# Performance work log

Measured on AMD Instinct MI355X. Metric: run time of the kernel, lower is better.

Reference implementation:

```python
import jax, jax.numpy as jnp
import numpy as np

D_MODEL = 768
N_HEADS = 12
D_K = D_MODEL // N_HEADS
NEG_INF = -1e10


def setup_inputs() -> dict:
    key = jax.random.key(0)
    ks = jax.random.split(key, 12)
    B, S = 2, 4096
    scale = 1.0 / np.sqrt(D_MODEL)
    inp = {
        "q": jax.random.normal(ks[0], (B, S, D_MODEL), jnp.float32),
        "k": jax.random.normal(ks[1], (B, S, D_MODEL), jnp.float32),
        "v": jax.random.normal(ks[2], (B, S, D_MODEL), jnp.float32),
        "mask": jnp.ones((B, S), jnp.int32),
        "Wq": jax.random.normal(ks[3], (D_MODEL, D_MODEL), jnp.float32) * scale,
        "bq": jnp.zeros((D_MODEL,), jnp.float32),
        "Wk": jax.random.normal(ks[4], (D_MODEL, D_MODEL), jnp.float32) * scale,
        "bk": jnp.zeros((D_MODEL,), jnp.float32),
        "Wv": jax.random.normal(ks[5], (D_MODEL, D_MODEL), jnp.float32) * scale,
        "bv": jnp.zeros((D_MODEL,), jnp.float32),
        "Wo": jax.random.normal(ks[6], (D_MODEL, D_MODEL), jnp.float32) * scale,
        "bo": jnp.zeros((D_MODEL,), jnp.float32),
    }
    return inp


def reference(q, k, v, mask, Wq, bq, Wk, bk, Wv, bv, Wo, bo):
    B, Sq, _ = q.shape
    Sk = k.shape[1]
    # linear projections (flax Linear: x @ kernel + bias)
    query = q @ Wq + bq
    key_ = k @ Wk + bk
    value = v @ Wv + bv
    # split heads: [B, H, S, d_k]
    query = query.reshape(B, Sq, N_HEADS, D_K).transpose(0, 2, 1, 3)
    key_ = key_.reshape(B, Sk, N_HEADS, D_K).transpose(0, 2, 1, 3)
    value = value.reshape(B, Sk, N_HEADS, D_K).transpose(0, 2, 1, 3)
    # scores [B, H, Sq, Sk]
    scores = jnp.einsum('bhqd,bhkd->bhqk', query, key_) / jnp.sqrt(
        jnp.asarray(D_K, query.dtype))
    m = mask[:, None, None, :]  # 2D mask -> [B,1,1,Sk]
    scores = jnp.where(m == 0, NEG_INF, scores)
    attn = jax.nn.softmax(scores, axis=-1)
    # dropout deterministic (is_training=False): identity
    x = jnp.einsum('bhqk,bhkd->bhqd', attn, value)
    x = x.transpose(0, 2, 1, 3).reshape(B, Sq, D_MODEL)
    return x @ Wo + bo
```

## Files before the change

### kernel.cpp

```cpp
#include <hip/hip_runtime.h>

typedef __attribute__((ext_vector_type(8))) short short8;
typedef __attribute__((ext_vector_type(4))) float floatx4;
typedef __attribute__((ext_vector_type(16))) float floatx16;
typedef unsigned short ushort_t;

#define S_LEN 4096
#define NH 12
#define DK 64
#define DM 768
#define BQ 128
#define LOG2E 1.4426950408889634f

static __device__ __forceinline__ unsigned short f2bf(float f) {
    unsigned int u = __float_as_uint(f);
    u += 0x7FFFu + ((u >> 16) & 1u);
    return (unsigned short)(u >> 16);
}
static __device__ __forceinline__ unsigned pack2(float a, float b) {
    return (unsigned)f2bf(a) | ((unsigned)f2bf(b) << 16);
}
static __device__ __forceinline__ void gld_lds16(const void* g, void* l) {
    __builtin_amdgcn_global_load_lds(
        (__attribute__((address_space(1))) void*)g,
        (__attribute__((address_space(3))) void*)l, 16, 0, 0);
}

__global__ __launch_bounds__(256)
void wtrans_kernel(const float* __restrict__ W0, const float* __restrict__ W1,
                   const float* __restrict__ W2, const float* __restrict__ W3,
                   ushort_t* __restrict__ T0, ushort_t* __restrict__ T1,
                   ushort_t* __restrict__ T2, ushort_t* __restrict__ T3) {
    __shared__ float tile[32][33];
    const int z = blockIdx.z;
    const float* W = (z == 0) ? W0 : (z == 1) ? W1 : (z == 2) ? W2 : W3;
    ushort_t* T = (z == 0) ? T0 : (z == 1) ? T1 : (z == 2) ? T2 : T3;
    const int bx = blockIdx.x, by = blockIdx.y;
    const int tx = threadIdx.x, ty = threadIdx.y;
    #pragma unroll
    for (int j = 0; j < 32; j += 8)
        tile[ty + j][tx] = W[(size_t)(by * 32 + ty + j) * DM + bx * 32 + tx];
    __syncthreads();
    #pragma unroll
    for (int j = 0; j < 32; j += 8)
        T[(size_t)(bx * 32 + ty + j) * DM + by * 32 + tx] = f2bf(tile[tx][ty + j]);
}

__global__ __launch_bounds__(256)
void cvt_kernel(const float* __restrict__ A0, const float* __restrict__ A1,
                const float* __restrict__ A2, ushort_t* __restrict__ O0,
                ushort_t* __restrict__ O1, ushort_t* __restrict__ O2) {
    const int z = blockIdx.y;
    const float* A = (z == 0) ? A0 : (z == 1) ? A1 : A2;
    ushort_t* O = (z == 0) ? O0 : (z == 1) ? O1 : O2;
    const size_t i = ((size_t)blockIdx.x * 256 + threadIdx.x) * 8;
    const float4 f0 = *(const float4*)(A + i);
    const float4 f1 = *(const float4*)(A + i + 4);
    uint4 o;
    o.x = pack2(f0.x, f0.y);
    o.y = pack2(f0.z, f0.w);
    o.z = pack2(f1.x, f1.y);
    o.w = pack2(f1.z, f1.w);
    *(uint4*)(O + i) = o;
}

__global__ __launch_bounds__(256)
void vtrans_kernel(const ushort_t* __restrict__ Vn, ushort_t* __restrict__ Vt) {
    __shared__ ushort_t tl[64 * 72];
    const int s0 = blockIdx.x * 64;
    const size_t bh = blockIdx.y;
    const int t = threadIdx.x;
    {
        const int r = t >> 2, c0 = (t & 3) * 16;
        const uint4* src = (const uint4*)(Vn + (bh * S_LEN + s0 + r) * DK + c0);
        uint4 a0 = src[0], a1 = src[1];
        uint4* dst = (uint4*)&tl[r * 72 + c0];
        dst[0] = a0;
        dst[1] = a1;
    }
    __syncthreads();
    {
        const int d = t >> 2, c0 = (t & 3) * 16;
        alignas(16) ushort_t tmp[16];
        #pragma unroll
        for (int j = 0; j < 16; ++j) tmp[j] = tl[(c0 + j) * 72 + d];
        uint4* dst = (uint4*)(Vt + (bh * DK + d) * S_LEN + s0 + c0);
        dst[0] = *(const uint4*)&tmp[0];
        dst[1] = *(const uint4*)&tmp[8];
    }
}

struct GemmArgs {
    const ushort_t* A[3];
    const ushort_t* Wt[3];
    const float* bias[3];
    void* C[3];
    float scale[3];
};

template <int MODE>
__global__ __launch_bounds__(256, 3)
void gemm_kernel(GemmArgs args) {
    __shared__ ushort_t As[128 * 32];
    __shared__ ushort_t Bs[128 * 32];
    const int z = blockIdx.z;
    const ushort_t* A = args.A[z];
    const ushort_t* Wt = args.Wt[z];
    const float* bias = args.bias[z];
    void* Carg = args.C[z];
    const float scale = args.scale[z];

    const int m0 = blockIdx.x * 128;
    const int n0 = blockIdx.y * 128;
    const int t = threadIdx.x;
    const int w = t >> 6, lane = t & 63, l15 = lane & 15, quad = lane >> 4;
    const int rowoff = (w >> 1) * 64, coloff = (w & 1) * 64;
    const int srow = w * 16 + (lane >> 2);
    const int scol = (lane & 3) * 8;

    floatx4 acc[4][4];
    #pragma unroll
    for (int i = 0; i < 4; ++i)
        #pragma unroll
        for (int j = 0; j < 4; ++j) acc[i][j] = (floatx4){0.f, 0.f, 0.f, 0.f};

    for (int kt = 0; kt < DM; kt += 32) {
        __syncthreads();
        #pragma unroll
        for (int j = 0; j < 2; ++j) {
            const int r = j * 64 + srow;
            gld_lds16(A + (size_t)(m0 + r) * DM + kt + scol, &As[r * 32 + scol]);
            gld_lds16(Wt + (size_t)(n0 + r) * DM + kt + scol, &Bs[r * 32 + scol]);
        }
        __asm__ __volatile__("s_waitcnt vmcnt(0)" ::: "memory");
        __syncthreads();
        short8 af[4], bfr[4];
        #pragma unroll
        for (int i = 0; i < 4; ++i)
            af[i] = *(const short8*)&As[(rowoff + 16 * i + l15) * 32 + quad * 8];
        #pragma unroll
        for (int j = 0; j < 4; ++j)
            bfr[j] = *(const short8*)&Bs[(coloff + 16 * j + l15) * 32 + quad * 8];
        #pragma unroll
        for (int i = 0; i < 4; ++i)
            #pragma unroll
            for (int j = 0; j < 4; ++j)
                acc[i][j] = __builtin_amdgcn_mfma_f32_16x16x32_bf16(af[i], bfr[j], acc[i][j], 0, 0, 0);
    }

    #pragma unroll
    for (int i = 0; i < 4; ++i) {
        #pragma unroll
        for (int j = 0; j < 4; ++j) {
            #pragma unroll
            for (int reg = 0; reg < 4; ++reg) {
                const int m = m0 + rowoff + 16 * i + quad * 4 + reg;
                const int n = n0 + coloff + 16 * j + l15;
                const float v2 = (acc[i][j][reg] + bias[n]) * scale;
                if (MODE == 0) {
                    ushort_t* Out = (ushort_t*)Carg;
                    const int b = m >> 12, s = m & 4095, h = n >> 6, d = n & 63;
                    Out[((size_t)((b * NH + h) * S_LEN + s)) * DK + d] = f2bf(v2);
                } else {
                    float* Out = (float*)Carg;
                    Out[(size_t)m * DM + n] = v2;
                }
            }
        }
    }
}

__global__ __launch_bounds__(256, 3)
void attn_kernel(const ushort_t* __restrict__ Q, const ushort_t* __restrict__ K,
                 const ushort_t* __restrict__ VT, const int* __restrict__ mask,
                 ushort_t* __restrict__ X) {
    __shared__ ushort_t Qs[BQ * DK];
    __shared__ ushort_t Ks0[64 * DK], Ks1[64 * DK];
    __shared__ ushort_t Vs0[64 * DK], Vs1[64 * DK];

    const int id = blockIdx.x;
    const int per = id >> 3;
    const int bh = (id & 7) * 3 + (per >> 5);
    const int qb = per & 31;
    const int b = bh / NH, h = bh - b * NH;
    const size_t bho = (size_t)bh * S_LEN;
    const ushort_t* Vbase = VT + (size_t)bh * DK * S_LEN;
    const int t = threadIdx.x;
    const int w = t >> 6, lane = t & 63, l31 = lane & 31, half = lane >> 5;
    const int q0 = qb * BQ;
    const int swl = l31 & 7;
    const int frow8 = lane >> 3;
    const int fcc = lane & 7;

    auto fillK = [&](int kv0, ushort_t* Kb) {
        #pragma unroll
        for (int j = 0; j < 2; ++j) {
            const int r = (w * 2 + j) * 8 + frow8;
            const int c8 = fcc ^ (r & 7);
            gld_lds16(K + (bho + kv0 + r) * DK + c8 * 8, &Kb[r * DK + fcc * 8]);
        }
    };
    auto fillV = [&](int kv0, ushort_t* Vb) {
        #pragma unroll
        for (int j = 0; j < 2; ++j) {
            const int r = (w * 2 + j) * 8 + frow8;
            const int c8 = fcc ^ (r & 7);
            gld_lds16(Vbase + (size_t)r * S_LEN + kv0 + c8 * 8, &Vb[r * DK + fcc * 8]);
        }
    };

    fillK(0, Ks0);
    fillV(0, Vs0);
    #pragma unroll
    for (int j = 0; j < 4; ++j) {
        const int r = (w * 4 + j) * 8 + frow8;
        const int c8 = fcc ^ (r & 7);
        gld_lds16(Q + (bho + q0 + r) * DK + c8 * 8, &Qs[r * DK + fcc * 8]);
    }
    int ok = 1;
    {
        const int* mrow = mask + (size_t)b * S_LEN + t * 16;
        #pragma unroll
        for (int i = 0; i < 4; ++i) {
            const int4 mm = *(const int4*)(mrow + i * 4);
            ok &= (mm.x != 0) & (mm.y != 0) & (mm.z != 0) & (mm.w != 0);
        }
    }
    const int allones = __syncthreads_and(ok);

    short8 qf[4];
    #pragma unroll
    for (int ks = 0; ks < 4; ++ks) {
        const int c8 = ks * 2 + half;
        qf[ks] = *(const short8*)&Qs[(w * 32 + l31) * DK + ((c8 ^ swl) << 3)];
    }

    floatx16 o[2];
    #pragma unroll
    for (int dt = 0; dt < 2; ++dt)
        #pragma unroll
        for (int r = 0; r < 16; ++r) o[dt][r] = 0.f;
    float l_r = 0.f;

    auto body = [&](int it, const ushort_t* Kc, const ushort_t* Vc,
                    ushort_t* Kn, ushort_t* Vn) {
        __syncthreads();
        if (it + 1 < S_LEN / 64) {
            fillK((it + 1) * 64, Kn);
            fillV((it + 1) * 64, Vn);
        }
        unsigned long long mb = ~0ULL;
        if (!allones) {
            const int mv = mask[(size_t)b * S_LEN + it * 64 + lane];
            mb = __ballot(mv != 0);
        }

        floatx16 st[2];
        __builtin_amdgcn_s_setprio(1);
        #pragma unroll
        for (int kt = 0; kt < 2; ++kt) {
            floatx16 s;
            #pragma unroll
            for (int r = 0; r < 16; ++r) s[r] = 0.f;
            #pragma unroll
            for (int ks = 0; ks < 4; ++ks) {
                const int c8 = ks * 2 + half;
                const short8 kf = *(const short8*)&Kc[(kt * 32 + l31) * DK + ((c8 ^ swl) << 3)];
                s = __builtin_amdgcn_mfma_f32_32x32x16_bf16(kf, qf[ks], s, 0, 0, 0);
            }
            st[kt] = s;
        }
        __builtin_amdgcn_s_setprio(0);

        if (mb != ~0ULL) {
            #pragma unroll
            for (int kt = 0; kt < 2; ++kt) {
                const unsigned bits = (unsigned)(mb >> (kt * 32));
                const unsigned vbits = bits >> (half * 4);
                #pragma unroll
                for (int r = 0; r < 16; ++r)
                    if (!((vbits >> ((r & 3) + 8 * (r >> 2))) & 1)) st[kt][r] = -3.0e10f;
            }
        }

        short8 pf[4];
        #pragma unroll
        for (int kt = 0; kt < 2; ++kt) {
            float p[16];
            #pragma unroll
            for (int r = 0; r < 16; ++r) p[r] = __builtin_amdgcn_exp2f(st[kt][r]);
            #pragma unroll
            for (int g = 0; g < 4; ++g)
                l_r += (p[4 * g + 0] + p[4 * g + 1]) + (p[4 * g + 2] + p[4 * g + 3]);
            unsigned c0[4], c1[4];
            #pragma unroll
            for (int g = 0; g < 4; ++g) {
                asm("v_cvt_pk_bf16_f32 %0, %1, %2"
                    : "=v"(c0[g]) : "v"(p[4 * g + 0]), "v"(p[4 * g + 1]));
                asm("v_cvt_pk_bf16_f32 %0, %1, %2"
                    : "=v"(c1[g]) : "v"(p[4 * g + 2]), "v"(p[4 * g + 3]));
            }
            asm("v_permlane32_swap_b32 %0, %1" : "+v"(c0[0]), "+v"(c0[1]));
            asm("v_permlane32_swap_b32 %0, %1" : "+v"(c1[0]), "+v"(c1[1]));
            asm("v_permlane32_swap_b32 %0, %1" : "+v"(c0[2]), "+v"(c0[3]));
            asm("v_permlane32_swap_b32 %0, %1" : "+v"(c1[2]), "+v"(c1[3]));
            union { short8 s8; unsigned u[4]; } w0, w1;
            w0.u[0] = c0[0]; w0.u[1] = c1[0]; w0.u[2] = c0[1]; w0.u[3] = c1[1];
            w1.u[0] = c0[2]; w1.u[1] = c1[2]; w1.u[2] = c0[3]; w1.u[3] = c1[3];
            pf[kt * 2 + 0] = w0.s8;
            pf[kt * 2 + 1] = w1.s8;
        }

        __builtin_amdgcn_s_setprio(1);
        #pragma unroll
        for (int dt = 0; dt < 2; ++dt) {
            #pragma unroll
            for (int ks = 0; ks < 4; ++ks) {
                const int c8 = ks * 2 + half;
                const short8 vf = *(const short8*)&Vc[(dt * 32 + l31) * DK + ((c8 ^ swl) << 3)];
                o[dt] = __builtin_amdgcn_mfma_f32_32x32x16_bf16(pf[ks], vf, o[dt], 0, 0, 0);
            }
        }
        __builtin_amdgcn_s_setprio(0);
    };

    for (int it = 0; it < S_LEN / 64; it += 2) {
        body(it, Ks0, Vs0, Ks1, Vs1);
        body(it + 1, Ks1, Vs1, Ks0, Vs0);
    }

    l_r += __shfl_xor(l_r, 32);
    const float inv = 1.0f / l_r;
    float iv[16];
    #pragma unroll
    for (int r = 0; r < 16; ++r)
        iv[r] = __shfl(inv, (r & 3) + 8 * (r >> 2) + 4 * half);
    #pragma unroll
    for (int dt = 0; dt < 2; ++dt)
        #pragma unroll
        for (int r = 0; r < 16; ++r) {
            const int qrow = (r & 3) + 8 * (r >> 2) + 4 * half;
            const int s = q0 + w * 32 + qrow;
            const int d = h * DK + dt * 32 + l31;
            X[((size_t)b * S_LEN + s) * DM + d] = f2bf(o[dt][r] * iv[r]);
        }
}

extern "C" void kernel_launch(void* const* d_in, const int* in_sizes, int n_in,
                              void* d_out, int out_size, void* d_ws, size_t ws_size,
                              hipStream_t stream) {
    const float* q = (const float*)d_in[0];
    const float* k = (const float*)d_in[1];
    const float* v = (const float*)d_in[2];
    const int* mask = (const int*)d_in[3];
    const float* Wq = (const float*)d_in[4];
    const float* bq = (const float*)d_in[5];
    const float* Wk = (const float*)d_in[6];
    const float* bk = (const float*)d_in[7];
    const float* Wv = (const float*)d_in[8];
    const float* bv = (const float*)d_in[9];
    const float* Wo = (const float*)d_in[10];
    const float* bo = (const float*)d_in[11];
    float* out = (float*)d_out;

    const size_t ME = (size_t)2 * S_LEN * DM;
    const size_t WE = (size_t)DM * DM;
    ushort_t* Qb = (ushort_t*)d_ws;
    ushort_t* Kb = Qb + ME;
    ushort_t* Vb = Kb + ME;
    ushort_t* VTb = Vb + ME;
    ushort_t* Xb = VTb + ME;
    ushort_t* Wqt = Xb + ME;
    ushort_t* Wkt = Wqt + WE;
    ushort_t* Wvt = Wkt + WE;
    ushort_t* Wot = Wvt + WE;
    ushort_t* Qa = Xb;
    ushort_t* Ka = VTb;
    ushort_t* Va = (ushort_t*)d_out;

    wtrans_kernel<<<dim3(DM / 32, DM / 32, 4), dim3(32, 8), 0, stream>>>(
        Wq, Wk, Wv, Wo, Wqt, Wkt, Wvt, Wot);

    cvt_kernel<<<dim3((int)(ME / 8 / 256), 3), 256, 0, stream>>>(q, k, v, Qa, Ka, Va);

    GemmArgs g1;
    g1.A[0] = Qa;  g1.A[1] = Ka;  g1.A[2] = Va;
    g1.Wt[0] = Wqt; g1.Wt[1] = Wkt; g1.Wt[2] = Wvt;
    g1.bias[0] = bq; g1.bias[1] = bk; g1.bias[2] = bv;
    g1.C[0] = Qb;  g1.C[1] = Kb;  g1.C[2] = Vb;
    g1.scale[0] = 0.125f * LOG2E;
    g1.scale[1] = 1.0f; g1.scale[2] = 1.0f;
    gemm_kernel<0><<<dim3((2 * S_LEN) / 128, DM / 128, 3), 256, 0, stream>>>(g1);

    vtrans_kernel<<<dim3(S_LEN / 64, 2 * NH), 256, 0, stream>>>(Vb, VTb);

    attn_kernel<<<dim3(768), 256, 0, stream>>>(Qb, Kb, VTb, mask, Xb);

    GemmArgs g2;
    g2.A[0] = Xb;  g2.A[1] = Xb;  g2.A[2] = Xb;
    g2.Wt[0] = Wot; g2.Wt[1] = Wot; g2.Wt[2] = Wot;
    g2.bias[0] = bo; g2.bias[1] = bo; g2.bias[2] = bo;
    g2.C[0] = out; g2.C[1] = out; g2.C[2] = out;
    g2.scale[0] = 1.0f; g2.scale[1] = 1.0f; g2.scale[2] = 1.0f;
    gemm_kernel<1><<<dim3((2 * S_LEN) / 128, DM / 128, 1), 256, 0, stream>>>(g2);
}
```

Before: 321.8 us.

## Fuse fp32-to-bf16 input conversion into QKV GEMM and swizzle LDS tiles

Removes the separate cvt_kernel and has the QKV projection GEMM load fp32 activations straight into LDS, converting them to bf16 with v_cvt_pk_bf16_f32 when fragments are read. Both A and B LDS tiles now use an XOR swizzle on the 16-byte chunk index to cut bank conflicts. In attention, the first MFMA of each score tile takes a zero accumulator instead of clearing registers first. This saves a full read and write pass over the three activation tensors, at the cost of doubling A-tile LDS traffic and adding conversion work inside the GEMM, which also lowers the occupancy headroom.

```diff
diff --git a/kernel.cpp b/kernel.cpp
--- a/kernel.cpp
+++ b/kernel.cpp
@@ -16,9 +16,6 @@
     unsigned int u = __float_as_uint(f);
     u += 0x7FFFu + ((u >> 16) & 1u);
     return (unsigned short)(u >> 16);
-}
-static __device__ __forceinline__ unsigned pack2(float a, float b) {
-    return (unsigned)f2bf(a) | ((unsigned)f2bf(b) << 16);
 }
 static __device__ __forceinline__ void gld_lds16(const void* g, void* l) {
     __builtin_amdgcn_global_load_lds(
@@ -44,24 +41,6 @@
     #pragma unroll
     for (int j = 0; j < 32; j += 8)
         T[(size_t)(bx * 32 + ty + j) * DM + by * 32 + tx] = f2bf(tile[tx][ty + j]);
-}
-
-__global__ __launch_bounds__(256)
-void cvt_kernel(const float* __restrict__ A0, const float* __restrict__ A1,
-                const float* __restrict__ A2, ushort_t* __restrict__ O0,
-                ushort_t* __restrict__ O1, ushort_t* __restrict__ O2) {
-    const int z = blockIdx.y;
-    const float* A = (z == 0) ? A0 : (z == 1) ? A1 : A2;
-    ushort_t* O = (z == 0) ? O0 : (z == 1) ? O1 : O2;
-    const size_t i = ((size_t)blockIdx.x * 256 + threadIdx.x) * 8;
-    const float4 f0 = *(const float4*)(A + i);
-    const float4 f1 = *(const float4*)(A + i + 4);
-    uint4 o;
-    o.x = pack2(f0.x, f0.y);
-    o.y = pack2(f0.z, f0.w);
-    o.z = pack2(f1.x, f1.y);
-    o.w = pack2(f1.z, f1.w);
-    *(uint4*)(O + i) = o;
 }
 
 __global__ __launch_bounds__(256)
@@ -91,20 +70,19 @@
 }
 
 struct GemmArgs {
-    const ushort_t* A[3];
+    const void* A[3];
     const ushort_t* Wt[3];
     const float* bias[3];
     void* C[3];
     float scale[3];
 };
 
-template <int MODE>
+template <int MODE, int AF32>
 __global__ __launch_bounds__(256, 3)
 void gemm_kernel(GemmArgs args) {
-    __shared__ ushort_t As[128 * 32];
-    __shared__ ushort_t Bs[128 * 32];
+    __shared__ __align__(16) ushort_t AsRaw[AF32 ? 128 * 32 * 2 : 128 * 32];
+    __shared__ __align__(16) ushort_t Bs[128 * 32];
     const int z = blockIdx.z;
-    const ushort_t* A = args.A[z];
     const ushort_t* Wt = args.Wt[z];
     const float* bias = args.bias[z];
     void* Carg = args.C[z];
@@ -115,8 +93,6 @@
     const int t = threadIdx.x;
     const int w = t >> 6, lane = t & 63, l15 = lane & 15, quad = lane >> 4;
     const int rowoff = (w >> 1) * 64, coloff = (w & 1) * 64;
-    const int srow = w * 16 + (lane >> 2);
-    const int scol = (lane & 3) * 8;
 
     floatx4 acc[4][4];
     #pragma unroll
@@ -126,21 +102,65 @@
 
     for (int kt = 0; kt < DM; kt += 32) {
         __syncthreads();
+        if (AF32) {
+            const float* Af = (const float*)args.A[z];
+            #pragma unroll
+            for (int j = 0; j < 4; ++j) {
+                const int r = (w * 4 + j) * 8 + (lane >> 3);
+                const int c = lane & 7;
+                const int sc = (((c >> 1) ^ (r & 3)) << 1) | (c & 1);
+                gld_lds16(Af + (size_t)(m0 + r) * DM + kt + sc * 4,
+                          (float*)AsRaw + r * 32 + c * 4);
+            }
+        } else {
+            const ushort_t* Ab = (const ushort_t*)args.A[z];
+            #pragma unroll
+            for (int j = 0; j < 2; ++j) {
+                const int r = j * 64 + w * 16 + (lane >> 2);
+                const int c = lane & 3;
+                const int sc = c ^ (r & 3);
+                gld_lds16(Ab + (size_t)(m0 + r) * DM + kt + sc * 8,
+                          &AsRaw[r * 32 + c * 8]);
+            }
+        }
         #pragma unroll
         for (int j = 0; j < 2; ++j) {
-            const int r = j * 64 + srow;
-            gld_lds16(A + (size_t)(m0 + r) * DM + kt + scol, &As[r * 32 + scol]);
-            gld_lds16(Wt + (size_t)(n0 + r) * DM + kt + scol, &Bs[r * 32 + scol]);
+            const int r = j * 64 + w * 16 + (lane >> 2);
+            const int c = lane & 3;
+            const int sc = c ^ (r & 3);
+            gld_lds16(Wt + (size_t)(n0 + r) * DM + kt + sc * 8,
+                      &Bs[r * 32 + c * 8]);
         }
         __asm__ __volatile__("s_waitcnt vmcnt(0)" ::: "memory");
         __syncthreads();
+
         short8 af[4], bfr[4];
-        #pragma unroll
-        for (int i = 0; i < 4; ++i)
-            af[i] = *(const short8*)&As[(rowoff + 16 * i + l15) * 32 + quad * 8];
-        #pragma unroll
-        for (int j = 0; j < 4; ++j)
-            bfr[j] = *(const short8*)&Bs[(coloff + 16 * j + l15) * 32 + quad * 8];
+        if (AF32) {
+            #pragma unroll
+            for (int i = 0; i < 4; ++i) {
+                const int r = rowoff + 16 * i + l15;
+                const float* rp = (const float*)AsRaw + r * 32 + ((quad ^ (r & 3)) * 8);
+                const float4 fa = *(const float4*)rp;
+                const float4 fb = *(const float4*)(rp + 4);
+                union { short8 s8; unsigned u[4]; } tt;
+                asm("v_cvt_pk_bf16_f32 %0, %1, %2" : "=v"(tt.u[0]) : "v"(fa.x), "v"(fa.y));
+                asm("v_cvt_pk_bf16_f32 %0, %1, %2" : "=v"(tt.u[1]) : "v"(fa.z), "v"(fa.w));
+                asm("v_cvt_pk_bf16_f32 %0, %1, %2" : "=v"(tt.u[2]) : "v"(fb.x), "v"(fb.y));
+                asm("v_cvt_pk_bf16_f32 %0, %1, %2" : "=v"(tt.u[3]) : "v"(fb.z), "v"(fb.w));
+                af[i] = tt.s8;
+            }
+        } else {
+            #pragma unroll
+            for (int i = 0; i < 4; ++i) {
+                const int r = rowoff + 16 * i + l15;
+                af[i] = *(const short8*)&AsRaw[r * 32 + ((quad ^ (r & 3)) * 8)];
+            }
+        }
+        #pragma unroll
+        for (int j = 0; j < 4; ++j) {
+            const int r = coloff + 16 * j + l15;
+            bfr[j] = *(const short8*)&Bs[r * 32 + ((quad ^ (r & 3)) * 8)];
+        }
         #pragma unroll
         for (int i = 0; i < 4; ++i)
             #pragma unroll
@@ -240,6 +260,9 @@
     for (int dt = 0; dt < 2; ++dt)
         #pragma unroll
         for (int r = 0; r < 16; ++r) o[dt][r] = 0.f;
+    floatx16 zv;
+    #pragma unroll
+    for (int r = 0; r < 16; ++r) zv[r] = 0.f;
     float l_r = 0.f;
 
     auto body = [&](int it, const ushort_t* Kc, const ushort_t* Vc,
@@ -260,10 +283,13 @@
         #pragma unroll
         for (int kt = 0; kt < 2; ++kt) {
             floatx16 s;
-            #pragma unroll
-            for (int r = 0; r < 16; ++r) s[r] = 0.f;
-            #pragma unroll
-            for (int ks = 0; ks < 4; ++ks) {
+            {
+                const int c8 = half;
+                const short8 kf = *(const short8*)&Kc[(kt * 32 + l31) * DK + ((c8 ^ swl) << 3)];
+                s = __builtin_amdgcn_mfma_f32_32x32x16_bf16(kf, qf[0], zv, 0, 0, 0);
+            }
+            #pragma unroll
+            for (int ks = 1; ks < 4; ++ks) {
                 const int c8 = ks * 2 + half;
                 const short8 kf = *(const short8*)&Kc[(kt * 32 + l31) * DK + ((c8 ^ swl) << 3)];
                 s = __builtin_amdgcn_mfma_f32_32x32x16_bf16(kf, qf[ks], s, 0, 0, 0);
@@ -374,23 +400,18 @@
     ushort_t* Wkt = Wqt + WE;
     ushort_t* Wvt = Wkt + WE;
     ushort_t* Wot = Wvt + WE;
-    ushort_t* Qa = Xb;
-    ushort_t* Ka = VTb;
-    ushort_t* Va = (ushort_t*)d_out;
 
     wtrans_kernel<<<dim3(DM / 32, DM / 32, 4), dim3(32, 8), 0, stream>>>(
         Wq, Wk, Wv, Wo, Wqt, Wkt, Wvt, Wot);
 
-    cvt_kernel<<<dim3((int)(ME / 8 / 256), 3), 256, 0, stream>>>(q, k, v, Qa, Ka, Va);
-
     GemmArgs g1;
-    g1.A[0] = Qa;  g1.A[1] = Ka;  g1.A[2] = Va;
+    g1.A[0] = q;   g1.A[1] = k;   g1.A[2] = v;
     g1.Wt[0] = Wqt; g1.Wt[1] = Wkt; g1.Wt[2] = Wvt;
     g1.bias[0] = bq; g1.bias[1] = bk; g1.bias[2] = bv;
     g1.C[0] = Qb;  g1.C[1] = Kb;  g1.C[2] = Vb;
     g1.scale[0] = 0.125f * LOG2E;
     g1.scale[1] = 1.0f; g1.scale[2] = 1.0f;
-    gemm_kernel<0><<<dim3((2 * S_LEN) / 128, DM / 128, 3), 256, 0, stream>>>(g1);
+    gemm_kernel<0, 1><<<dim3((2 * S_LEN) / 128, DM / 128, 3), 256, 0, stream>>>(g1);
 
     vtrans_kernel<<<dim3(S_LEN / 64, 2 * NH), 256, 0, stream>>>(Vb, VTb);
 
@@ -402,5 +423,5 @@
     g2.bias[0] = bo; g2.bias[1] = bo; g2.bias[2] = bo;
     g2.C[0] = out; g2.C[1] = out; g2.C[2] = out;
     g2.scale[0] = 1.0f; g2.scale[1] = 1.0f; g2.scale[2] = 1.0f;
-    gemm_kernel<1><<<dim3((2 * S_LEN) / 128, DM / 128, 1), 256, 0, stream>>>(g2);
-}
+    gemm_kernel<1, 0><<<dim3((2 * S_LEN) / 128, DM / 128, 1), 256, 0, stream>>>(g2);
+}
```

Measured after the change: 335.0 us. +4.1%, slower.
